# Kernel tuning notes

Hardware: AMD Instinct MI355X
Metric: run time of the kernel (lower is better)

The kernel has to match this reference:

```python
import jax, jax.numpy as jnp
import numpy as np

BIT_WIDTH = 8
UP = float(2 ** (BIT_WIDTH - 1) - 1)   # 127
LOW = float(-(2 ** (BIT_WIDTH - 1)))   # -128


def setup_inputs() -> dict:
    key = jax.random.key(0)
    k1, k2, k3, k4, k5 = jax.random.split(key, 5)
    B, Cin, H, W = 32, 256, 56, 56
    Cout, kH, kW = 256, 3, 3
    x = jax.random.normal(k1, (B, Cin, H, W), dtype=jnp.float32)
    weight = jax.random.normal(k2, (Cout, Cin, kH, kW), dtype=jnp.float32) * 0.05
    bias = jax.random.normal(k3, (Cout,), dtype=jnp.float32) * 0.1
    # positive quantization scales (roughly map |w|~0.15, |x|~3 into int8 range)
    sw = jax.random.uniform(k4, (Cout,), minval=200.0, maxval=800.0, dtype=jnp.float32)
    sx = jax.random.uniform(k5, (1,), minval=20.0, maxval=40.0, dtype=jnp.float32)
    return {"x": x, "weight": weight, "bias": bias, "sw": sw, "sx": sx}


def reference(x, weight, bias, sw, sx):
    """QConv2d forward in q_inference (quant-simulation) mode:
    per-out-channel fake-quantize weight, per-tensor fake-quantize input,
    then float conv2d + bias. jnp.round matches torch.round (half-to-even)."""
    swb = sw[:, None, None, None]                      # [Cout,1,1,1]
    q_w = jnp.round(jnp.clip(weight * swb, LOW, UP)) / swb
    q_x = jnp.round(jnp.clip(x * sx[0], LOW, UP)) / sx[0]
    out = jax.lax.conv_general_dilated(
        q_x, q_w,
        window_strides=(1, 1),
        padding=((1, 1), (1, 1)),
        dimension_numbers=("NCHW", "OIHW", "NCHW"),
    )
    return out + bias[None, :, None, None]
```

## Files before the change

### kernel.cpp

```cpp
#include <hip/hip_runtime.h>
#include <stdint.h>

typedef int int32x4 __attribute__((ext_vector_type(4)));

#define HW_        3136
#define CHW_       802816
#define HP_        58
#define WP_        58
#define PLANE_PIX  107648ull
#define PLANE_B    (PLANE_PIX*16)
#define QXP_BYTES  (16ull*PLANE_B)
#define QWT_BYTES  (9ull*16*256*16)

__device__ __forceinline__ signed char quant8(float v, float s) {
    float t = v * s;
    t = fmaxf(t, -128.0f);
    t = fminf(t, 127.0f);
    return (signed char)(int)rintf(t);
}

__global__ __launch_bounds__(256) void halo_rows_kernel(signed char* __restrict__ qxp2) {
    int idx = blockIdx.x*256 + threadIdx.x;
    if (idx < 16*32*2*58) {
        int cq = idx / (32*2*58);
        int r  = idx % (32*2*58);
        int b  = r / (2*58);
        int t  = r % (2*58);
        int hp = (t / 58) * (HP_-1);
        int wp = t % 58;
        *(int32x4*)(qxp2 + ((size_t)cq*PLANE_PIX + (size_t)(b*HP_+hp)*WP_ + wp)*16)
            = (int32x4){0,0,0,0};
    }
}

__global__ __launch_bounds__(256) void quant_w_kernel(
    const float* __restrict__ wgt, const float* __restrict__ sw,
    signed char* __restrict__ qwT2)
{
    __shared__ __align__(16) signed char lw[9*272];
    const int o = blockIdx.x, c = threadIdx.x;
    const float s = sw[o];
    const float* wp = wgt + ((size_t)o*256 + c)*9;
    #pragma unroll
    for (int kk = 0; kk < 9; ++kk)
        lw[kk*272 + c] = quant8(wp[kk], s);
    __syncthreads();
    if (c < 144) {
        int kk = c / 16, cq = c - kk*16;
        int32x4 v = *(const int32x4*)&lw[kk*272 + cq*16];
        *(int32x4*)(qwT2 + ((size_t)(kk*16 + cq)*256 + o)*16) = v;
    }
}

__global__ __launch_bounds__(256) void quant_x_kernel(
    const float* __restrict__ x, const float* __restrict__ sx,
    signed char* __restrict__ qxp2)
{
    const int tid = threadIdx.x;
    const int bh = blockIdx.x;
    const int b = bh / 56, h = bh % 56;
    const float s = sx[0];
    if (tid < 224) {
        const int w  = tid % 56;
        const int cg = tid / 56;
        const size_t xrow = (size_t)b*CHW_ + (size_t)h*56 + w;
        const size_t pb = ((size_t)(b*HP_ + h + 1)*WP_ + 1 + w)*16;
        #pragma unroll
        for (int k = 0; k < 4; ++k) {
            const int cq = cg*4 + k;
            const float* xp = x + xrow + (size_t)(cq*16)*HW_;
            int pk[4];
            #pragma unroll
            for (int g = 0; g < 4; ++g) {
                int b0 = (unsigned char)quant8(xp[(size_t)(4*g+0)*HW_], s);
                int b1 = (unsigned char)quant8(xp[(size_t)(4*g+1)*HW_], s);
                int b2 = (unsigned char)quant8(xp[(size_t)(4*g+2)*HW_], s);
                int b3 = (unsigned char)quant8(xp[(size_t)(4*g+3)*HW_], s);
                pk[g] = b0 | (b1 << 8) | (b2 << 16) | (b3 << 24);
            }
            *(int32x4*)(qxp2 + (size_t)cq*PLANE_B + pb) = (int32x4){pk[0],pk[1],pk[2],pk[3]};
        }
    } else {
        int t2 = tid - 224;
        int cq = t2 >> 1, wp = (t2 & 1) * (WP_-1);
        const size_t rowpix = (size_t)(b*HP_ + h + 1)*WP_;
        *(int32x4*)(qxp2 + ((size_t)cq*PLANE_PIX + rowpix + wp)*16) = (int32x4){0,0,0,0};
    }
}

__device__ __forceinline__ void load16_lds(const void* g, void* l) {
    __builtin_amdgcn_global_load_lds(
        (const unsigned int*)g,
        reinterpret_cast<__attribute__((address_space(3))) unsigned int*>(
            reinterpret_cast<uintptr_t>(l)),
        16, 0, 0);
}

__global__ __launch_bounds__(256, 2) void conv_kernel(
    const signed char* __restrict__ qxp2, const signed char* __restrict__ qwT2,
    const float* __restrict__ sw, const float* __restrict__ bias,
    const float* __restrict__ sx, float* __restrict__ out)
{
    __shared__ __align__(16) signed char smem[65536];

    const int tid  = threadIdx.x;
    const int wave = tid >> 6;
    const int lane = tid & 63;
    const int quad = lane >> 4;
    const int l15  = lane & 15;

    const int bid = blockIdx.x;
    const int swz = (bid & 7) * 196 + (bid >> 3);
    const int s0  = (swz >> 1) * 128;
    const int o0  = (swz & 1) * 128;

    const unsigned sp0 = (unsigned)(s0 + lane);
    const unsigned sp1 = (unsigned)(s0 + 64 + lane);
    unsigned b0 = sp0 / HW_, r0 = sp0 - b0*HW_;
    unsigned b1 = sp1 / HW_, r1 = sp1 - b1*HW_;
    unsigned h0 = r0 / 56,   w0 = r0 - h0*56;
    unsigned h1 = r1 / 56,   w1 = r1 - h1*56;
    const size_t bOff0 = ((size_t)(b0*HP_ + h0)*WP_ + w0)*16;
    const size_t bOff1 = ((size_t)(b1*HP_ + h1)*WP_ + w1)*16;
    const size_t aOff0 = (size_t)(o0 + lane)*16;
    const size_t aOff1 = aOff0 + 1024;

    int32x4 acc[4][4];
    #pragma unroll
    for (int i = 0; i < 4; ++i)
        #pragma unroll
        for (int j = 0; j < 4; ++j)
            acc[i][j] = (int32x4){0,0,0,0};

    const int wo = (wave & 1) << 6;
    const int wn = (wave >> 1) << 6;

    auto stage = [&](int st, signed char* bufA, signed char* bufB) {
        const int kk  = st >> 1;
        const int cq0 = (st & 1) * 8;
        const size_t kshift = (size_t)((kk/3)*WP_ + (kk%3))*16;
        const size_t aKK = (size_t)kk*16*4096;
        #pragma unroll
        for (int t = 0; t < 2; ++t) {
            const int kc = 2*wave + t;
            const int cq = cq0 + kc;
            const signed char* aG = qwT2 + aKK + (size_t)cq*4096;
            load16_lds(aG + aOff0, bufA + kc*2048);
            load16_lds(aG + aOff1, bufA + kc*2048 + 1024);
            const signed char* bG = qxp2 + (size_t)cq*PLANE_B + kshift;
            load16_lds(bG + bOff0, bufB + kc*2048);
            load16_lds(bG + bOff1, bufB + kc*2048 + 1024);
        }
    };

    stage(0, smem, smem + 16384);

    for (int st = 0; st < 18; ++st) {
        signed char* ldsA = smem + ((st & 1) << 15);
        signed char* ldsB = ldsA + 16384;
        if (st < 17) {
            signed char* nb = smem + (((st + 1) & 1) << 15);
            stage(st + 1, nb, nb + 16384);
            asm volatile("s_waitcnt vmcnt(8)");
        } else {
            asm volatile("s_waitcnt vmcnt(0)");
        }
        __builtin_amdgcn_s_barrier();
        __builtin_amdgcn_sched_barrier(0);
        #pragma unroll
        for (int ks = 0; ks < 2; ++ks) {
            const int ck = (ks*4 + quad)*2048;
            int32x4 af[4], bf[4];
            #pragma unroll
            for (int t = 0; t < 4; ++t) {
                af[t] = *(const int32x4*)&ldsA[ck + (wo + t*16 + l15)*16];
                bf[t] = *(const int32x4*)&ldsB[ck + (wn + t*16 + l15)*16];
            }
            __builtin_amdgcn_s_setprio(1);
            #pragma unroll
            for (int mt = 0; mt < 4; ++mt)
                #pragma unroll
                for (int nt = 0; nt < 4; ++nt)
                    acc[mt][nt] = __builtin_amdgcn_mfma_i32_16x16x64_i8(
                        af[mt], bf[nt], acc[mt][nt], 0, 0, 0);
            __builtin_amdgcn_s_setprio(0);
        }
        __builtin_amdgcn_sched_barrier(0);
        __builtin_amdgcn_s_barrier();
    }
    asm volatile("" ::: "memory");

    float* lt    = (float*)smem;
    float* invS  = (float*)(smem + 33792);
    float* biasS = (float*)(smem + 34304);
    if (tid < 128) {
        float s = sw[o0 + tid];
        invS[tid]  = 1.0f / (s * sx[0]);
        biasS[tid] = bias[o0 + tid];
    }
    #pragma unroll
    for (int p = 0; p < 2; ++p) {
        __syncthreads();
        if ((wave & 1) == p) {
            #pragma unroll
            for (int mt = 0; mt < 4; ++mt)
                #pragma unroll
                for (int nt = 0; nt < 4; ++nt)
                    #pragma unroll
                    for (int r = 0; r < 4; ++r)
                        lt[(mt*16 + quad*4 + r)*132 + wn + nt*16 + l15]
                            = (float)acc[mt][nt][r];
        }
        __syncthreads();
        #pragma unroll
        for (int i = 0; i < 8; ++i) {
            int idx = i*256 + tid;
            int o = idx >> 5;
            int c = idx & 31;
            float4 v = *(const float4*)&lt[o*132 + 4*c];
            int ol = p*64 + o;
            float is = invS[ol], bs = biasS[ol];
            unsigned sp = (unsigned)(s0 + 4*c);
            unsigned b  = sp / HW_;
            unsigned pos = sp - b*HW_;
            float4 wv;
            wv.x = fmaf(v.x, is, bs); wv.y = fmaf(v.y, is, bs);
            wv.z = fmaf(v.z, is, bs); wv.w = fmaf(v.w, is, bs);
            *(float4*)(out + (size_t)b*CHW_ + (size_t)(o0 + ol)*HW_ + pos) = wv;
        }
    }
}

extern "C" void kernel_launch(void* const* d_in, const int* in_sizes, int n_in,
                              void* d_out, int out_size, void* d_ws, size_t ws_size,
                              hipStream_t stream)
{
    (void)in_sizes; (void)n_in; (void)out_size; (void)ws_size;
    const float* x    = (const float*)d_in[0];
    const float* wgt  = (const float*)d_in[1];
    const float* bias = (const float*)d_in[2];
    const float* sw   = (const float*)d_in[3];
    const float* sx   = (const float*)d_in[4];
    float* out = (float*)d_out;

    signed char* qxp2 = (signed char*)d_ws;
    signed char* qwT2 = qxp2 + QXP_BYTES;

    halo_rows_kernel<<<232, 256, 0, stream>>>(qxp2);
    quant_w_kernel<<<256, 256, 0, stream>>>(wgt, sw, qwT2);
    quant_x_kernel<<<1792, 256, 0, stream>>>(x, sx, qxp2);
    conv_kernel<<<1568, 256, 0, stream>>>(qxp2, qwT2, sw, bias, sx, out);
}
```

Before: 271.2 us.

## Load weight fragments directly into registers, keep only input tile in LDS

Result: no change. 267.0 us (-1.5%).

```diff
diff --git a/kernel.cpp b/kernel.cpp
--- a/kernel.cpp
+++ b/kernel.cpp
@@ -96,12 +96,57 @@
         16, 0, 0);
 }
 
+#define LOADA(st, AF) {                                                        \
+    const signed char* aG_ = qwT2 + (size_t)((st) >> 1)*65536                  \
+                           + (size_t)(((st) & 1) * 8)*4096 + aRowQ;            \
+    AF[0] = *(const int32x4*)(aG_ +     0);                                    \
+    AF[1] = *(const int32x4*)(aG_ +   256);                                    \
+    AF[2] = *(const int32x4*)(aG_ +   512);                                    \
+    AF[3] = *(const int32x4*)(aG_ +   768);                                    \
+    AF[4] = *(const int32x4*)(aG_ + 16384);                                    \
+    AF[5] = *(const int32x4*)(aG_ + 16640);                                    \
+    AF[6] = *(const int32x4*)(aG_ + 16896);                                    \
+    AF[7] = *(const int32x4*)(aG_ + 17152);                                    \
+}
+
+#define STEP(st, AFC, AFN, LAST) {                                             \
+    signed char* ldsB_ = smem + (((st) & 1) << 14);                            \
+    if (!(LAST)) {                                                             \
+        stageB((st) + 1, smem + ((((st) + 1) & 1) << 14));                     \
+        LOADA((st) + 1, AFN);                                                  \
+        __builtin_amdgcn_sched_barrier(0);                                     \
+        asm volatile("s_waitcnt vmcnt(12)");                                   \
+    } else {                                                                   \
+        asm volatile("s_waitcnt vmcnt(0)");                                    \
+    }                                                                          \
+    __builtin_amdgcn_s_barrier();                                              \
+    __builtin_amdgcn_sched_barrier(0);                                         \
+    _Pragma("unroll")                                                          \
+    for (int ks = 0; ks < 2; ++ks) {                                           \
+        const int ck = (ks*4 + quad)*2048;                                     \
+        int32x4 bf[4];                                                         \
+        _Pragma("unroll")                                                      \
+        for (int t = 0; t < 4; ++t)                                            \
+            bf[t] = *(const int32x4*)&ldsB_[ck + (wn + t*16 + l15)*16];        \
+        __builtin_amdgcn_s_setprio(1);                                         \
+        _Pragma("unroll")                                                      \
+        for (int mt = 0; mt < 4; ++mt)                                         \
+            _Pragma("unroll")                                                  \
+            for (int nt = 0; nt < 4; ++nt)                                     \
+                acc[mt][nt] = __builtin_amdgcn_mfma_i32_16x16x64_i8(           \
+                    AFC[ks*4 + mt], bf[nt], acc[mt][nt], 0, 0, 0);             \
+        __builtin_amdgcn_s_setprio(0);                                         \
+    }                                                                          \
+    __builtin_amdgcn_sched_barrier(0);                                         \
+    __builtin_amdgcn_s_barrier();                                              \
+}
+
 __global__ __launch_bounds__(256, 2) void conv_kernel(
     const signed char* __restrict__ qxp2, const signed char* __restrict__ qwT2,
     const float* __restrict__ sw, const float* __restrict__ bias,
     const float* __restrict__ sx, float* __restrict__ out)
 {
-    __shared__ __align__(16) signed char smem[65536];
+    __shared__ __align__(16) signed char smem[34816];
 
     const int tid  = threadIdx.x;
     const int wave = tid >> 6;
@@ -122,8 +167,10 @@
     unsigned h1 = r1 / 56,   w1 = r1 - h1*56;
     const size_t bOff0 = ((size_t)(b0*HP_ + h0)*WP_ + w0)*16;
     const size_t bOff1 = ((size_t)(b1*HP_ + h1)*WP_ + w1)*16;
-    const size_t aOff0 = (size_t)(o0 + lane)*16;
-    const size_t aOff1 = aOff0 + 1024;
+
+    const int wo = (wave & 1) << 6;
+    const int wn = (wave >> 1) << 6;
+    const size_t aRowQ = (size_t)quad*4096 + (size_t)(o0 + wo + l15)*16;
 
     int32x4 acc[4][4];
     #pragma unroll
@@ -132,62 +179,32 @@
         for (int j = 0; j < 4; ++j)
             acc[i][j] = (int32x4){0,0,0,0};
 
-    const int wo = (wave & 1) << 6;
-    const int wn = (wave >> 1) << 6;
-
-    auto stage = [&](int st, signed char* bufA, signed char* bufB) {
+    auto stageB = [&](int st, signed char* bufB) {
         const int kk  = st >> 1;
         const int cq0 = (st & 1) * 8;
         const size_t kshift = (size_t)((kk/3)*WP_ + (kk%3))*16;
-        const size_t aKK = (size_t)kk*16*4096;
         #pragma unroll
         for (int t = 0; t < 2; ++t) {
             const int kc = 2*wave + t;
-            const int cq = cq0 + kc;
-            const signed char* aG = qwT2 + aKK + (size_t)cq*4096;
-            load16_lds(aG + aOff0, bufA + kc*2048);
-            load16_lds(aG + aOff1, bufA + kc*2048 + 1024);
-            const signed char* bG = qxp2 + (size_t)cq*PLANE_B + kshift;
+            const signed char* bG = qxp2 + (size_t)(cq0 + kc)*PLANE_B + kshift;
             load16_lds(bG + bOff0, bufB + kc*2048);
             load16_lds(bG + bOff1, bufB + kc*2048 + 1024);
         }
     };
 
-    stage(0, smem, smem + 16384);
-
-    for (int st = 0; st < 18; ++st) {
-        signed char* ldsA = smem + ((st & 1) << 15);
-        signed char* ldsB = ldsA + 16384;
-        if (st < 17) {
-            signed char* nb = smem + (((st + 1) & 1) << 15);
-            stage(st + 1, nb, nb + 16384);
-            asm volatile("s_waitcnt vmcnt(8)");
-        } else {
-            asm volatile("s_waitcnt vmcnt(0)");
-        }
-        __builtin_amdgcn_s_barrier();
-        __builtin_amdgcn_sched_barrier(0);
-        #pragma unroll
-        for (int ks = 0; ks < 2; ++ks) {
-            const int ck = (ks*4 + quad)*2048;
-            int32x4 af[4], bf[4];
-            #pragma unroll
-            for (int t = 0; t < 4; ++t) {
-                af[t] = *(const int32x4*)&ldsA[ck + (wo + t*16 + l15)*16];
-                bf[t] = *(const int32x4*)&ldsB[ck + (wn + t*16 + l15)*16];
-            }
-            __builtin_amdgcn_s_setprio(1);
-            #pragma unroll
-            for (int mt = 0; mt < 4; ++mt)
-                #pragma unroll
-                for (int nt = 0; nt < 4; ++nt)
-                    acc[mt][nt] = __builtin_amdgcn_mfma_i32_16x16x64_i8(
-                        af[mt], bf[nt], acc[mt][nt], 0, 0, 0);
-            __builtin_amdgcn_s_setprio(0);
-        }
-        __builtin_amdgcn_sched_barrier(0);
-        __builtin_amdgcn_s_barrier();
-    }
+    int32x4 aP[8], aQ[8];
+    stageB(0, smem);
+    LOADA(0, aP);
+
+    #pragma unroll 1
+    for (int s2 = 0; s2 < 8; ++s2) {
+        const int st0 = 2*s2;
+        STEP(st0,     aP, aQ, false);
+        STEP(st0 + 1, aQ, aP, false);
+    }
+    STEP(16, aP, aQ, false);
+    STEP(17, aQ, aP, true);
+
     asm volatile("" ::: "memory");
 
     float* lt    = (float*)smem;
```

## Load conv weights directly to registers, triple-buffer input in LDS, merge prep kernels

Applied to the files above, without the earlier changes.

Result: faster. 263.9 us (-2.7%).

```diff
diff --git a/kernel.cpp b/kernel.cpp
--- a/kernel.cpp
+++ b/kernel.cpp
@@ -19,46 +19,32 @@
     return (signed char)(int)rintf(t);
 }
 
-__global__ __launch_bounds__(256) void halo_rows_kernel(signed char* __restrict__ qxp2) {
-    int idx = blockIdx.x*256 + threadIdx.x;
-    if (idx < 16*32*2*58) {
-        int cq = idx / (32*2*58);
-        int r  = idx % (32*2*58);
-        int b  = r / (2*58);
-        int t  = r % (2*58);
-        int hp = (t / 58) * (HP_-1);
-        int wp = t % 58;
-        *(int32x4*)(qxp2 + ((size_t)cq*PLANE_PIX + (size_t)(b*HP_+hp)*WP_ + wp)*16)
-            = (int32x4){0,0,0,0};
-    }
-}
-
-__global__ __launch_bounds__(256) void quant_w_kernel(
+__global__ __launch_bounds__(256) void prep_kernel(
+    const float* __restrict__ x, const float* __restrict__ sx,
     const float* __restrict__ wgt, const float* __restrict__ sw,
-    signed char* __restrict__ qwT2)
+    signed char* __restrict__ qxp2, signed char* __restrict__ qwT2)
 {
     __shared__ __align__(16) signed char lw[9*272];
-    const int o = blockIdx.x, c = threadIdx.x;
-    const float s = sw[o];
-    const float* wp = wgt + ((size_t)o*256 + c)*9;
-    #pragma unroll
-    for (int kk = 0; kk < 9; ++kk)
-        lw[kk*272 + c] = quant8(wp[kk], s);
-    __syncthreads();
-    if (c < 144) {
-        int kk = c / 16, cq = c - kk*16;
-        int32x4 v = *(const int32x4*)&lw[kk*272 + cq*16];
-        *(int32x4*)(qwT2 + ((size_t)(kk*16 + cq)*256 + o)*16) = v;
-    }
-}
-
-__global__ __launch_bounds__(256) void quant_x_kernel(
-    const float* __restrict__ x, const float* __restrict__ sx,
-    signed char* __restrict__ qxp2)
-{
     const int tid = threadIdx.x;
-    const int bh = blockIdx.x;
-    const int b = bh / 56, h = bh % 56;
+    const int blk = blockIdx.x;
+
+    if (blk >= 1792) {
+        const int o = blk - 1792;
+        const float s = sw[o];
+        const float* wp = wgt + ((size_t)o*256 + tid)*9;
+        #pragma unroll
+        for (int kk = 0; kk < 9; ++kk)
+            lw[kk*272 + tid] = quant8(wp[kk], s);
+        __syncthreads();
+        if (tid < 144) {
+            int kk = tid / 16, cq = tid - kk*16;
+            int32x4 v = *(const int32x4*)&lw[kk*272 + cq*16];
+            *(int32x4*)(qwT2 + ((size_t)(kk*16 + cq)*256 + o)*16) = v;
+        }
+        return;
+    }
+
+    const int b = blk / 56, h = blk % 56;
     const float s = sx[0];
     if (tid < 224) {
         const int w  = tid % 56;
@@ -86,6 +72,16 @@
         const size_t rowpix = (size_t)(b*HP_ + h + 1)*WP_;
         *(int32x4*)(qxp2 + ((size_t)cq*PLANE_PIX + rowpix + wp)*16) = (int32x4){0,0,0,0};
     }
+    if (h == 0) {
+        for (int t = tid; t < 16*2*58; t += 256) {
+            int cq = t / 116;
+            int r  = t - cq*116;
+            int hp = (r / 58) * (HP_-1);
+            int wp = r % 58;
+            *(int32x4*)(qxp2 + ((size_t)cq*PLANE_PIX + (size_t)(b*HP_+hp)*WP_ + wp)*16)
+                = (int32x4){0,0,0,0};
+        }
+    }
 }
 
 __device__ __forceinline__ void load16_lds(const void* g, void* l) {
@@ -96,15 +92,59 @@
         16, 0, 0);
 }
 
-__global__ __launch_bounds__(256, 2) void conv_kernel(
+#define LOADA4(st, AF) {                                                      \
+    const signed char* aG_ = qwT2 + (size_t)(((st) >> 2)*65536                \
+                           + (((st) & 3)*4)*4096) + aRow;                     \
+    AF[0] = *(const int32x4*)(aG_ +   0);                                     \
+    AF[1] = *(const int32x4*)(aG_ + 256);                                     \
+    AF[2] = *(const int32x4*)(aG_ + 512);                                     \
+    AF[3] = *(const int32x4*)(aG_ + 768);                                     \
+}
+
+#define STAGEB(st) {                                                          \
+    const size_t ksh_ = (size_t)((((st) >> 2)/3)*WP_ + (((st) >> 2)%3))*16;   \
+    const signed char* bG_ = qxp2 + (size_t)(((st) & 3)*4)*PLANE_B            \
+                           + wOffB + ksh_;                                    \
+    signed char* dst_ = smem + ((st)%3)*8192 + dstW;                          \
+    load16_lds(bG_ + bOff0, dst_);                                            \
+    load16_lds(bG_ + bOff1, dst_ + 1024);                                     \
+}
+
+#define STEP(st, AC, AN) {                                                    \
+    if ((st) == 35) asm volatile("s_waitcnt vmcnt(4)");                       \
+    else            asm volatile("s_waitcnt vmcnt(6)");                       \
+    __builtin_amdgcn_s_barrier();                                             \
+    __builtin_amdgcn_sched_barrier(0);                                        \
+    if ((st) + 1 < 36) LOADA4((st) + 1, AN);                                  \
+    if ((st) + 2 < 36) STAGEB((st) + 2);                                      \
+    const signed char* bR_ = smem + ((st)%3)*8192;                            \
+    int32x4 bf[4];                                                            \
+    _Pragma("unroll")                                                         \
+    for (int t = 0; t < 4; ++t)                                               \
+        bf[t] = *(const int32x4*)&bR_[rdOff + t*256];                         \
+    __builtin_amdgcn_s_setprio(1);                                            \
+    _Pragma("unroll")                                                         \
+    for (int mt = 0; mt < 4; ++mt)                                            \
+        _Pragma("unroll")                                                     \
+        for (int nt = 0; nt < 4; ++nt)                                        \
+            acc[mt][nt] = __builtin_amdgcn_mfma_i32_16x16x64_i8(              \
+                AC[mt], bf[nt], acc[mt][nt], 0, 0, 0);                        \
+    __builtin_amdgcn_s_setprio(0);                                            \
+    __builtin_amdgcn_sched_barrier(0);                                        \
+}
+
+#define STEP2(s) STEP((s),   aP, aQ) STEP((s)+1, aQ, aP)
+#define STEP6(s) STEP2(s) STEP2((s)+2) STEP2((s)+4)
+
+__global__ __launch_bounds__(256, 3) void conv_kernel(
     const signed char* __restrict__ qxp2, const signed char* __restrict__ qwT2,
     const float* __restrict__ sw, const float* __restrict__ bias,
     const float* __restrict__ sx, float* __restrict__ out)
 {
-    __shared__ __align__(16) signed char smem[65536];
+    __shared__ __align__(16) signed char smem[34816];
 
     const int tid  = threadIdx.x;
-    const int wave = tid >> 6;
+    const int wv   = tid >> 6;
     const int lane = tid & 63;
     const int quad = lane >> 4;
     const int l15  = lane & 15;
@@ -122,8 +162,13 @@
     unsigned h1 = r1 / 56,   w1 = r1 - h1*56;
     const size_t bOff0 = ((size_t)(b0*HP_ + h0)*WP_ + w0)*16;
     const size_t bOff1 = ((size_t)(b1*HP_ + h1)*WP_ + w1)*16;
-    const size_t aOff0 = (size_t)(o0 + lane)*16;
-    const size_t aOff1 = aOff0 + 1024;
+
+    const int wo = (wv & 1) << 6;
+    const int wn = (wv >> 1) << 6;
+    const size_t aRow  = (size_t)quad*4096 + (size_t)(o0 + wo + l15)*16;
+    const size_t wOffB = (size_t)wv*PLANE_B;
+    const int    dstW  = wv*2048;
+    const int    rdOff = quad*2048 + (wn + l15)*16;
 
     int32x4 acc[4][4];
     #pragma unroll
@@ -132,62 +177,16 @@
         for (int j = 0; j < 4; ++j)
             acc[i][j] = (int32x4){0,0,0,0};
 
-    const int wo = (wave & 1) << 6;
-    const int wn = (wave >> 1) << 6;
-
-    auto stage = [&](int st, signed char* bufA, signed char* bufB) {
-        const int kk  = st >> 1;
-        const int cq0 = (st & 1) * 8;
-        const size_t kshift = (size_t)((kk/3)*WP_ + (kk%3))*16;
-        const size_t aKK = (size_t)kk*16*4096;
-        #pragma unroll
-        for (int t = 0; t < 2; ++t) {
-            const int kc = 2*wave + t;
-            const int cq = cq0 + kc;
-            const signed char* aG = qwT2 + aKK + (size_t)cq*4096;
-            load16_lds(aG + aOff0, bufA + kc*2048);
-            load16_lds(aG + aOff1, bufA + kc*2048 + 1024);
-            const signed char* bG = qxp2 + (size_t)cq*PLANE_B + kshift;
-            load16_lds(bG + bOff0, bufB + kc*2048);
-            load16_lds(bG + bOff1, bufB + kc*2048 + 1024);
-        }
-    };
-
-    stage(0, smem, smem + 16384);
-
-    for (int st = 0; st < 18; ++st) {
-        signed char* ldsA = smem + ((st & 1) << 15);
-        signed char* ldsB = ldsA + 16384;
-        if (st < 17) {
-            signed char* nb = smem + (((st + 1) & 1) << 15);
-            stage(st + 1, nb, nb + 16384);
-            asm volatile("s_waitcnt vmcnt(8)");
-        } else {
-            asm volatile("s_waitcnt vmcnt(0)");
-        }
-        __builtin_amdgcn_s_barrier();
-        __builtin_amdgcn_sched_barrier(0);
-        #pragma unroll
-        for (int ks = 0; ks < 2; ++ks) {
-            const int ck = (ks*4 + quad)*2048;
-            int32x4 af[4], bf[4];
-            #pragma unroll
-            for (int t = 0; t < 4; ++t) {
-                af[t] = *(const int32x4*)&ldsA[ck + (wo + t*16 + l15)*16];
-                bf[t] = *(const int32x4*)&ldsB[ck + (wn + t*16 + l15)*16];
-            }
-            __builtin_amdgcn_s_setprio(1);
-            #pragma unroll
-            for (int mt = 0; mt < 4; ++mt)
-                #pragma unroll
-                for (int nt = 0; nt < 4; ++nt)
-                    acc[mt][nt] = __builtin_amdgcn_mfma_i32_16x16x64_i8(
-                        af[mt], bf[nt], acc[mt][nt], 0, 0, 0);
-            __builtin_amdgcn_s_setprio(0);
-        }
-        __builtin_amdgcn_sched_barrier(0);
-        __builtin_amdgcn_s_barrier();
-    }
+    int32x4 aP[4], aQ[4];
+
+    STAGEB(0);
+    STAGEB(1);
+    __builtin_amdgcn_sched_barrier(0);
+    LOADA4(0, aP);
+    __builtin_amdgcn_sched_barrier(0);
+
+    STEP6(0) STEP6(6) STEP6(12) STEP6(18) STEP6(24) STEP6(30)
+
     asm volatile("" ::: "memory");
 
     float* lt    = (float*)smem;
@@ -201,7 +200,7 @@
     #pragma unroll
     for (int p = 0; p < 2; ++p) {
         __syncthreads();
-        if ((wave & 1) == p) {
+        if ((wv & 1) == p) {
             #pragma unroll
             for (int mt = 0; mt < 4; ++mt)
                 #pragma unroll
@@ -223,10 +222,10 @@
             unsigned sp = (unsigned)(s0 + 4*c);
             unsigned b  = sp / HW_;
             unsigned pos = sp - b*HW_;
-            float4 wv;
-            wv.x = fmaf(v.x, is, bs); wv.y = fmaf(v.y, is, bs);
-            wv.z = fmaf(v.z, is, bs); wv.w = fmaf(v.w, is, bs);
-            *(float4*)(out + (size_t)b*CHW_ + (size_t)(o0 + ol)*HW_ + pos) = wv;
+            float4 wv4;
+            wv4.x = fmaf(v.x, is, bs); wv4.y = fmaf(v.y, is, bs);
+            wv4.z = fmaf(v.z, is, bs); wv4.w = fmaf(v.w, is, bs);
+            *(float4*)(out + (size_t)b*CHW_ + (size_t)(o0 + ol)*HW_ + pos) = wv4;
         }
     }
 }
@@ -246,8 +245,6 @@
     signed char* qxp2 = (signed char*)d_ws;
     signed char* qwT2 = qxp2 + QXP_BYTES;
 
-    halo_rows_kernel<<<232, 256, 0, stream>>>(qxp2);
-    quant_w_kernel<<<256, 256, 0, stream>>>(wgt, sw, qwT2);
-    quant_x_kernel<<<1792, 256, 0, stream>>>(x, sx, qxp2);
+    prep_kernel<<<2048, 256, 0, stream>>>(x, sx, wgt, sw, qxp2, qwT2);
     conv_kernel<<<1568, 256, 0, stream>>>(qxp2, qwT2, sw, bias, sx, out);
 }
```
